# Performance work log

Hardware: AMD Instinct MI355X
Metric: run time of the kernel (lower is better)

The kernel has to match this reference:

```python
import jax, jax.numpy as jnp
import numpy as np
from jax import lax

K = 32768          # queue size
C = 100            # num_classes == len(cls_num_list1)
B = 1024           # batch size (features.shape[0] - K)
D = 128            # embedding dim
ALPHA = 0.05; BETA = 1.0; GAMMA = 1.0; SUPT = 1.0
T = 0.07; BASE_T = 0.07   # base_temperature defaults to temperature
SMOOTH = 0.0; EPS = 1e-12


def setup_inputs() -> dict:
    key = jax.random.key(0)
    k1, k2, k3, k4 = jax.random.split(key, 4)
    features = jax.random.normal(k1, (B + K, D), dtype=jnp.float32)
    features = features / jnp.linalg.norm(features, axis=1, keepdims=True)  # contrastive feats are L2-normalized
    centers = jax.random.normal(k2, (C, D), dtype=jnp.float32)
    centers = centers / jnp.linalg.norm(centers, axis=1, keepdims=True)
    sup_logits = jax.random.normal(k3, (B, C), dtype=jnp.float32)
    labels = jax.random.randint(k4, (B + K,), 0, C, dtype=jnp.int32)
    return {"features": features, "sup_logits": sup_logits, "centers": centers, "labels": labels}


def _loss(features, sup_logits, centers, labels):
    f32 = features.dtype
    lab_c = jnp.arange(C, dtype=labels.dtype)
    lab1 = jnp.concatenate([labels[:B], lab_c])                 # [B+C]
    mask = (labels[:B, None] == labels[None, :]).astype(f32)    # [B, B+K]
    mask1 = (lab1[:B, None] == lab1[None, :]).astype(f32)       # [B, B+C]
    # class counts over batch+queue (batch_cls_count) and batch+centers (batch_cls_count1)
    cls_count = jnp.zeros((C,), f32).at[labels].add(1.0)
    cls_count1 = jnp.zeros((C,), f32).at[lab1].add(1.0)
    diag = jnp.arange(B)
    logits_mask = jnp.ones((B, B + K), f32).at[diag, diag].set(0.0)
    logits_mask1 = jnp.ones((B, B + C), f32).at[diag, diag].set(0.0)
    mask = mask * logits_mask
    mask1 = mask1 * logits_mask1

    # ---- branch 1: batch anchors vs [batch, class centers] ----
    feats1 = jnp.concatenate([features[:B], centers], axis=0)   # [B+C, D]
    logits1 = (features[:B] @ feats1.T) / T                     # [B, B+C]
    logits1 = logits1 - lax.stop_gradient(logits1.max(axis=1, keepdims=True))
    exp1 = jnp.exp(logits1) * logits_mask1
    w1 = cls_count1[lab1][None, :] - mask1                      # per-instance class weight
    denom1 = (exp1 / w1).sum(axis=1, keepdims=True)
    log_prob1 = logits1 - jnp.log(denom1 + EPS)
    loss1 = -jnp.mean((mask1 * log_prob1).sum(1) / mask1.sum(1))

    # ---- branch 2: [sup_logits, batch anchors vs batch+queue] ----
    adc = (features[:B] @ features.T) / T                       # [B, B+K]
    logits = jnp.concatenate([sup_logits / SUPT, adc], axis=1)  # [B, C+B+K] (self.weight is None)
    logits = logits - lax.stop_gradient(logits.max(axis=1, keepdims=True))
    one_hot = jax.nn.one_hot(labels[:B], C, dtype=f32)
    one_hot = SMOOTH / (C - 1) * (1.0 - one_hot) + (1.0 - SMOOTH) * one_hot
    mask_full = jnp.concatenate([one_hot * BETA, mask * ALPHA], axis=1)
    lmask_full = jnp.concatenate([jnp.ones((B, C), f32), GAMMA * logits_mask], axis=1)
    expl = jnp.exp(logits) * lmask_full
    lab_full = jnp.concatenate([lab_c, labels])                 # [C+B+K]
    w = cls_count[lab_full][None, :] - mask_full
    denom = (expl / w).sum(axis=1, keepdims=True)
    log_prob = logits - jnp.log(denom + EPS)
    loss2 = -(T / BASE_T) * jnp.mean((mask_full * log_prob).sum(1) / mask_full.sum(1))
    return loss1 + loss2


def reference(features, sup_logits, centers, labels):
    return _loss(features, sup_logits, centers, labels)
```

## Files before the change

kernel.cpp:

```cpp
#include <hip/hip_runtime.h>
#include <math.h>

#define KQ   32768
#define CC   100
#define BB   1024
#define DD   128
#define NTOT (BB + KQ)
#define CB_CENT 1056
#define NCB  1060
#define NPB  265
#define NHIST 33
#define NCG2 66
#define CG_SUP 75
#define NSL  75

#define INV_T  14.285714285714286f
#define K2E    20.609929f
#define ALPHA  0.05f
#define EPSV   1e-12f

typedef __attribute__((ext_vector_type(8)))  short          short8;
typedef __attribute__((ext_vector_type(8)))  unsigned short ushort8;
typedef __attribute__((ext_vector_type(16))) float          float16;

__device__ __forceinline__ unsigned short f2bf_rne(float f) {
    unsigned int u = __float_as_uint(f);
    return (unsigned short)((u + 0x7FFFu + ((u >> 16) & 1u)) >> 16);
}


__global__ __launch_bounds__(256) void prep_k(const float* __restrict__ feats,
                                              const float* __restrict__ centers,
                                              const int* __restrict__ labels,
                                              unsigned short* __restrict__ X2,
                                              int* __restrict__ cntP,
                                              int* __restrict__ cntB) {
    const int b = blockIdx.x, t = threadIdx.x;
    if (b >= NPB) {
        const int h = b - NPB;
        __shared__ int hA[CC], hB[CC];
        if (t < CC) { hA[t] = 0; hB[t] = 0; }
        __syncthreads();
        const int base = h * 1024;
#pragma unroll
        for (int q = 0; q < 4; ++q) {
            int l = labels[base + q * 256 + t];
            atomicAdd(&hA[l], 1);
            if (h == 0) atomicAdd(&hB[l], 1);
        }
        __syncthreads();
        if (t < 128) {
            cntP[h * 128 + t] = (t < CC) ? hA[t] : 0;
            if (h == 0) cntB[t] = (t < CC) ? hB[t] : 0;
        }
        return;
    }
    __shared__ unsigned short sm[8 * 66 * 8];
    const int rl = t >> 3, c8 = t & 7;
#pragma unroll
    for (int cbi = 0; cbi < 4; ++cbi) {
        const int cb = b * 4 + cbi;
        if (cb >= NCB) break;
        const int r = cb * 32 + rl;
        const float* src;
        if (r < NTOT)            src = &feats[(size_t)r * DD];
        else if (r < NTOT + CC)  src = &centers[(size_t)(r - NTOT) * DD];
        else                     src = nullptr;
        if (cbi) __syncthreads();
#pragma unroll
        for (int s = 0; s < 2; ++s) {
            const int c8p = c8 + 8 * s;
            float v[8];
            if (src) {
                const float4* p = (const float4*)(src + c8p * 8);
                float4 q0 = p[0], q1 = p[1];
                v[0]=q0.x; v[1]=q0.y; v[2]=q0.z; v[3]=q0.w;
                v[4]=q1.x; v[5]=q1.y; v[6]=q1.z; v[7]=q1.w;
            } else {
#pragma unroll
                for (int j = 0; j < 8; ++j) v[j] = 0.f;
            }
            ushort8 H;
#pragma unroll
            for (int m = 0; m < 8; ++m) H[m] = f2bf_rne(v[m]);
            const int ks = c8p >> 1, lh = c8p & 1;
            *(ushort8*)&sm[(ks * 66 + rl + 32 * lh) * 8] = H;
        }
        __syncthreads();
        ushort8* dst = (ushort8*)((char*)X2 + (size_t)cb * 8192);
#pragma unroll
        for (int j = 0; j < 2; ++j) {
            const int idx = j * 256 + t;
            const int ks = idx >> 6, ln = idx & 63;
            dst[idx] = *(const ushort8*)&sm[(ks * 66 + ln) * 8];
        }
    }
}

__device__ __forceinline__ void epi_tile(
    const float16& acc, int cb, int lc, float rn, float drm, bool checkDiag,
    int half, int ln, int growbase, const int* rlab, float* sS, float* sN)
{
    const int ccol = cb * 32 + ln;
#pragma unroll
    for (int reg = 0; reg < 16; ++reg) {
        int ro = (reg & 3) + 8 * (reg >> 2) + 4 * half;
        float a  = acc[reg];
        float mf = (lc == rlab[reg]) ? 1.f : 0.f;
        float wgt = fmaf(mf, drm, rn);
        if (checkDiag) {
            bool d = (ccol == growbase + ro);
            wgt = d ? 0.f : wgt;
            mf  = d ? 0.f : mf;
        }
        float e = exp2f(fmaf(a, K2E, -K2E));
        sS[reg] = fmaf(e, wgt, sS[reg]);
        sN[reg] = fmaf(mf, a, sN[reg]);
    }
}

__device__ __forceinline__ void pair_tiles(
    const char* Xb, int cb0, int cb1,
    int lc0, float rn0, float drm0, bool dg0,
    int lc1, float rn1, float drm1, bool dg1,
    int lane, int half, int ln, int growbase,
    const short8* Ah, const int* rlab, float* sS, float* sN)
{
    const size_t b0 = (size_t)cb0 * 8192 + (size_t)lane * 16;
    const size_t b1 = (size_t)cb1 * 8192 + (size_t)lane * 16;
    float16 a0, a1;
#pragma unroll
    for (int reg = 0; reg < 16; ++reg) { a0[reg] = 0.f; a1[reg] = 0.f; }
#pragma unroll
    for (int ks = 0; ks < 8; ++ks) {
        short8 B0 = *(const short8*)(Xb + b0 + (size_t)ks * 1024);
        short8 B1 = *(const short8*)(Xb + b1 + (size_t)ks * 1024);
        a0 = __builtin_amdgcn_mfma_f32_32x32x16_bf16(Ah[ks], B0, a0, 0, 0, 0);
        a1 = __builtin_amdgcn_mfma_f32_32x32x16_bf16(Ah[ks], B1, a1, 0, 0, 0);
    }
    epi_tile(a0, cb0, lc0, rn0, drm0, dg0, half, ln, growbase, rlab, sS, sN);
    epi_tile(a1, cb1, lc1, rn1, drm1, dg1, half, ln, growbase, rlab, sS, sN);
}

__global__ __launch_bounds__(256) void gemm_k(
    const unsigned short* __restrict__ X2, const int* __restrict__ labels,
    const int* __restrict__ cntP, const int* __restrict__ cntB,
    const float* __restrict__ sup,
    float* __restrict__ pS, float* __restrict__ pN,
    float* __restrict__ supS, float* __restrict__ supLi) {
    const int b = blockIdx.x;
    const int xcd = b & 7, l = b >> 3;
    const int rt = l & 7, ci = l >> 3;
    const int cg = xcd + 8 * ci;
    if (cg > CG_SUP) return;

    const int tid = threadIdx.x;
    const int lane = tid & 63, w = tid >> 6;
    const int half = lane >> 5, ln = lane & 31;
    const char* Xb = (const char*)X2;

    __shared__ float cntAF[128], rnA[128], drmA[128], rn1S[128], drm1S[128];
    if (tid < 128) {
        int s = 0;
#pragma unroll
        for (int h = 0; h < NHIST; ++h) s += cntP[h * 128 + tid];
        float cf = (float)s;
        cntAF[tid] = cf;
        rnA[tid] = (s > 0) ? __builtin_amdgcn_rcpf(cf) : 0.f;
        drmA[tid] = (s > 0) ? (__builtin_amdgcn_rcpf(cf - ALPHA) - rnA[tid]) : 0.f;
        int sb = cntB[tid];
        float c1 = (float)(sb + 1);
        float rn1 = __builtin_amdgcn_rcpf(c1);
        rn1S[tid] = rn1;
        drm1S[tid] = __builtin_amdgcn_rcpf(fmaxf(c1 - 1.f, 1.f)) - rn1;
    }
    __syncthreads();

    if (cg == CG_SUP) {
        const int g = rt * 4 + w;
        const int c0 = lane, c1 = lane + 64;
        float n0 = cntAF[c0];
        float rA0 = __builtin_amdgcn_rcpf(n0);
        float rAm0 = __builtin_amdgcn_rcpf(fmaxf(n0 - 1.f, 1.f));
        float rA1 = 0.f, rAm1 = 0.f;
        if (lane < 36) {
            float n1 = cntAF[c1];
            rA1 = __builtin_amdgcn_rcpf(n1);
            rAm1 = __builtin_amdgcn_rcpf(fmaxf(n1 - 1.f, 1.f));
        }
        for (int rr = 0; rr < 32; ++rr) {
            int row = g * 32 + rr;
            int li = labels[row];
            const float* srow = &sup[(size_t)row * CC];
            float v0 = srow[c0];
            float s = __expf(v0 - INV_T) * ((c0 == li) ? rAm0 : rA0);
            float liv = (c0 == li) ? v0 : 0.f;
            if (lane < 36) {
                float v1 = srow[c1];
                s += __expf(v1 - INV_T) * ((c1 == li) ? rAm1 : rA1);
                liv += (c1 == li) ? v1 : 0.f;
            }
#pragma unroll
            for (int off = 1; off < 64; off <<= 1) {
                s += __shfl_xor(s, off, 64);
                liv += __shfl_xor(liv, off, 64);
            }
            if (lane == 0) { supS[row] = s; supLi[row] = liv; }
        }
        return;
    }

    const int rb = rt * 4 + w;
    const int growbase = rt * 128 + w * 32;
    short8 Ah[8];
    {
        size_t abase = (size_t)rb * 8192 + (size_t)lane * 16;
#pragma unroll
        for (int ks = 0; ks < 8; ++ks)
            Ah[ks] = *(const short8*)(Xb + abase + (size_t)ks * 1024);
    }
    int rlab[16];
#pragma unroll
    for (int reg = 0; reg < 16; ++reg) {
        int ro = (reg & 3) + 8 * (reg >> 2) + 4 * half;
        rlab[reg] = labels[growbase + ro];
    }
    float sS[16], sN[16];
#pragma unroll
    for (int reg = 0; reg < 16; ++reg) { sS[reg] = 0.f; sN[reg] = 0.f; }

    const bool isB2 = (cg < NCG2);
    const int t1 = cg - NCG2;
    if (isB2) {
#pragma unroll
        for (int p = 0; p < 8; ++p) {
            const int cb0 = cg * 16 + 2 * p, cb1 = cb0 + 1;
            int lc0 = labels[cb0 * 32 + ln];
            int lc1 = labels[cb1 * 32 + ln];
            pair_tiles(Xb, cb0, cb1, lc0, rnA[lc0], drmA[lc0], cb0 == rb,
                       lc1, rnA[lc1], drmA[lc1], cb1 == rb,
                       lane, half, ln, growbase, Ah, rlab, sS, sN);
        }
    } else {
        const bool isBatch = (t1 < 8);
#pragma unroll
        for (int p = 0; p < 2; ++p) {
            int cb0, cb1, lc0, lc1;
            if (isBatch) {
                cb0 = t1 * 4 + 2 * p; cb1 = cb0 + 1;
                lc0 = labels[cb0 * 32 + ln];
                lc1 = labels[cb1 * 32 + ln];
            } else {
                cb0 = CB_CENT + 2 * p; cb1 = cb0 + 1;
                int q0 = cb0 * 32 + ln - NTOT, q1 = cb1 * 32 + ln - NTOT;
                lc0 = (q0 < CC) ? q0 : -1;
                lc1 = (q1 < CC) ? q1 : -1;
            }
            float rn0 = (lc0 >= 0) ? rn1S[lc0] : 0.f;
            float drm0 = (lc0 >= 0) ? drm1S[lc0] : 0.f;
            float rn1 = (lc1 >= 0) ? rn1S[lc1] : 0.f;
            float drm1 = (lc1 >= 0) ? drm1S[lc1] : 0.f;
            pair_tiles(Xb, cb0, cb1, lc0, rn0, drm0, isBatch && (cb0 == rb),
                       lc1, rn1, drm1, isBatch && (cb1 == rb),
                       lane, half, ln, growbase, Ah, rlab, sS, sN);
        }
    }
    const int slice = isB2 ? cg : (NCG2 + t1);
#pragma unroll
    for (int reg = 0; reg < 16; ++reg) {
        float a = sS[reg], c = sN[reg];
#pragma unroll
        for (int off = 1; off < 32; off <<= 1) {
            a += __shfl_xor(a, off, 64);
            c += __shfl_xor(c, off, 64);
        }
        if (ln == 0) {
            int ro = (reg & 3) + 8 * (reg >> 2) + 4 * half;
            int grow = growbase + ro;
            pS[(size_t)slice * BB + grow] = a;
            pN[(size_t)slice * BB + grow] = c;
        }
    }
}

__global__ __launch_bounds__(1024) void finalize_k(
    const int* __restrict__ labels,
    const int* __restrict__ cntP, const int* __restrict__ cntB,
    const float* __restrict__ pS, const float* __restrict__ pN,
    const float* __restrict__ supS, const float* __restrict__ supLi,
    float* __restrict__ out) {
    const int t = threadIdx.x;
    __shared__ float cntA[128];
    if (t < 128) {
        int s = 0;
#pragma unroll
        for (int h = 0; h < NHIST; ++h) s += cntP[h * 128 + t];
        cntA[t] = (float)s;
    }
    __syncthreads();
    const int li = labels[t];
    float S2 = supS[t], N2 = 0.f;
#pragma unroll 4
    for (int c = 0; c < NCG2; ++c) {
        S2 += pS[(size_t)c * BB + t];
        N2 += pN[(size_t)c * BB + t];
    }
    float S1 = 0.f, N1v = 0.f;
#pragma unroll
    for (int c = NCG2; c < NSL; ++c) {
        S1 += pS[(size_t)c * BB + t];
        N1v += pN[(size_t)c * BB + t];
    }
    N2 *= INV_T; N1v *= INV_T;
    float sli = supLi[t];
    float cA = cntA[li];
    float msum2 = fmaf(ALPHA, cA - 1.f, 1.f);
    float loss2 = -(fmaf(ALPHA, N2, sli) / msum2 - INV_T - logf(S2 + EPSV));
    float loss1 = -(N1v / (float)cntB[li] - INV_T - logf(S1 + EPSV));
    float s = loss1 + loss2;
    __shared__ float buf[16];
#pragma unroll
    for (int off = 1; off < 64; off <<= 1) s += __shfl_xor(s, off, 64);
    if ((t & 63) == 0) buf[t >> 6] = s;
    __syncthreads();
    if (t < 64) {
        float x = (t < 16) ? buf[t] : 0.f;
#pragma unroll
        for (int off = 1; off < 16; off <<= 1) x += __shfl_xor(x, off, 64);
        if (t == 0) out[0] = x / (float)BB;
    }
}

extern "C" void kernel_launch(void* const* d_in, const int* in_sizes, int n_in,
                              void* d_out, int out_size, void* d_ws, size_t ws_size,
                              hipStream_t stream) {
    const float* feats   = (const float*)d_in[0];
    const float* sup     = (const float*)d_in[1];
    const float* centers = (const float*)d_in[2];
    const int*   labels  = (const int*)d_in[3];
    float* out = (float*)d_out;
    char*  wsb = (char*)d_ws;

    const size_t X2_BYTES = (size_t)NCB * 8192;
    unsigned short* X2 = (unsigned short*)wsb;
    char* base2 = wsb + X2_BYTES;
    int* cntP = (int*)base2;
    int* cntB = cntP + NHIST * 128;
    float* pS = (float*)(cntB + 128);
    float* pN = pS + (size_t)NSL * BB;
    float* supS  = pN + (size_t)NSL * BB;
    float* supLi = supS + BB;

    prep_k<<<NPB + NHIST, 256, 0, stream>>>(feats, centers, labels, X2, cntP, cntB);
    gemm_k<<<8 * 8 * 10, 256, 0, stream>>>(X2, labels, cntP, cntB, sup,
                                           pS, pN, supS, supLi);
    finalize_k<<<1, 1024, 0, stream>>>(labels, cntP, cntB, pS, pN, supS, supLi, out);
}
```

Before: 130.3 us.

## Split GEMM into single-wave blocks, add class-weight table kernel, one chunk per prep block

The prep kernel now converts one 32-row chunk per block instead of four, which launches more blocks. A new tiny kernel computes the per-class reciprocal weight tables once, so GEMM blocks no longer each re-sum the histogram partials and synchronise. The GEMM kernel uses 64-thread blocks, each covering one row block and half as many column tiles, which doubles the column groups and the partial-sum slices. The goal is better load balance and less redundant preamble work, at the cost of an extra launch, more partial sums for finalize to reduce, and no A-fragment reuse across waves in a block.

```diff
diff --git a/kernel.cpp b/kernel.cpp
--- a/kernel.cpp
+++ b/kernel.cpp
@@ -8,11 +8,11 @@
 #define NTOT (BB + KQ)
 #define CB_CENT 1056
 #define NCB  1060
-#define NPB  265
 #define NHIST 33
-#define NCG2 66
-#define CG_SUP 75
-#define NSL  75
+#define NCG2 132
+#define CG_SUP 141
+#define NSL  141
+#define NCI  18
 
 #define INV_T  14.285714285714286f
 #define K2E    20.609929f
@@ -36,8 +36,8 @@
                                               int* __restrict__ cntP,
                                               int* __restrict__ cntB) {
     const int b = blockIdx.x, t = threadIdx.x;
-    if (b >= NPB) {
-        const int h = b - NPB;
+    if (b >= NCB) {
+        const int h = b - NCB;
         __shared__ int hA[CC], hB[CC];
         if (t < CC) { hA[t] = 0; hB[t] = 0; }
         __syncthreads();
@@ -56,45 +56,62 @@
         return;
     }
     __shared__ unsigned short sm[8 * 66 * 8];
+    const int cb = b;
     const int rl = t >> 3, c8 = t & 7;
-#pragma unroll
-    for (int cbi = 0; cbi < 4; ++cbi) {
-        const int cb = b * 4 + cbi;
-        if (cb >= NCB) break;
-        const int r = cb * 32 + rl;
-        const float* src;
-        if (r < NTOT)            src = &feats[(size_t)r * DD];
-        else if (r < NTOT + CC)  src = &centers[(size_t)(r - NTOT) * DD];
-        else                     src = nullptr;
-        if (cbi) __syncthreads();
-#pragma unroll
-        for (int s = 0; s < 2; ++s) {
-            const int c8p = c8 + 8 * s;
-            float v[8];
-            if (src) {
-                const float4* p = (const float4*)(src + c8p * 8);
-                float4 q0 = p[0], q1 = p[1];
-                v[0]=q0.x; v[1]=q0.y; v[2]=q0.z; v[3]=q0.w;
-                v[4]=q1.x; v[5]=q1.y; v[6]=q1.z; v[7]=q1.w;
-            } else {
-#pragma unroll
-                for (int j = 0; j < 8; ++j) v[j] = 0.f;
-            }
-            ushort8 H;
-#pragma unroll
-            for (int m = 0; m < 8; ++m) H[m] = f2bf_rne(v[m]);
-            const int ks = c8p >> 1, lh = c8p & 1;
-            *(ushort8*)&sm[(ks * 66 + rl + 32 * lh) * 8] = H;
-        }
-        __syncthreads();
-        ushort8* dst = (ushort8*)((char*)X2 + (size_t)cb * 8192);
-#pragma unroll
-        for (int j = 0; j < 2; ++j) {
-            const int idx = j * 256 + t;
-            const int ks = idx >> 6, ln = idx & 63;
-            dst[idx] = *(const ushort8*)&sm[(ks * 66 + ln) * 8];
-        }
-    }
+    const int r = cb * 32 + rl;
+    const float* src;
+    if (r < NTOT)            src = &feats[(size_t)r * DD];
+    else if (r < NTOT + CC)  src = &centers[(size_t)(r - NTOT) * DD];
+    else                     src = nullptr;
+#pragma unroll
+    for (int s = 0; s < 2; ++s) {
+        const int c8p = c8 + 8 * s;
+        float v[8];
+        if (src) {
+            const float4* p = (const float4*)(src + c8p * 8);
+            float4 q0 = p[0], q1 = p[1];
+            v[0]=q0.x; v[1]=q0.y; v[2]=q0.z; v[3]=q0.w;
+            v[4]=q1.x; v[5]=q1.y; v[6]=q1.z; v[7]=q1.w;
+        } else {
+#pragma unroll
+            for (int j = 0; j < 8; ++j) v[j] = 0.f;
+        }
+        ushort8 H;
+#pragma unroll
+        for (int m = 0; m < 8; ++m) H[m] = f2bf_rne(v[m]);
+        const int ks = c8p >> 1, lh = c8p & 1;
+        *(ushort8*)&sm[(ks * 66 + rl + 32 * lh) * 8] = H;
+    }
+    __syncthreads();
+    ushort8* dst = (ushort8*)((char*)X2 + (size_t)cb * 8192);
+#pragma unroll
+    for (int j = 0; j < 2; ++j) {
+        const int idx = j * 256 + t;
+        const int ks = idx >> 6, ln2 = idx & 63;
+        dst[idx] = *(const ushort8*)&sm[(ks * 66 + ln2) * 8];
+    }
+}
+
+__global__ __launch_bounds__(128) void tables_k(
+    const int* __restrict__ cntP, const int* __restrict__ cntB,
+    float2* __restrict__ wA, float2* __restrict__ w1, float2* __restrict__ wS,
+    float* __restrict__ cAf, int* __restrict__ cBi) {
+    const int t = threadIdx.x;
+    int s = 0;
+#pragma unroll
+    for (int h = 0; h < NHIST; ++h) s += cntP[h * 128 + t];
+    float cf = (float)s;
+    float rn = (s > 0) ? __builtin_amdgcn_rcpf(cf) : 0.f;
+    float dr = (s > 0) ? (__builtin_amdgcn_rcpf(cf - ALPHA) - rn) : 0.f;
+    wA[t] = make_float2(rn, dr);
+    wS[t] = make_float2(__builtin_amdgcn_rcpf(cf),
+                        __builtin_amdgcn_rcpf(fmaxf(cf - 1.f, 1.f)));
+    int sb = cntB[t];
+    float c1 = (float)(sb + 1);
+    float r1 = __builtin_amdgcn_rcpf(c1);
+    w1[t] = make_float2(r1, __builtin_amdgcn_rcpf(fmaxf(c1 - 1.f, 1.f)) - r1);
+    cAf[t] = cf;
+    cBi[t] = sb;
 }
 
 __device__ __forceinline__ void epi_tile(
@@ -142,54 +159,30 @@
     epi_tile(a1, cb1, lc1, rn1, drm1, dg1, half, ln, growbase, rlab, sS, sN);
 }
 
-__global__ __launch_bounds__(256) void gemm_k(
+__global__ __launch_bounds__(64, 4) void gemm_k(
     const unsigned short* __restrict__ X2, const int* __restrict__ labels,
-    const int* __restrict__ cntP, const int* __restrict__ cntB,
-    const float* __restrict__ sup,
+    const float2* __restrict__ wA, const float2* __restrict__ w1,
+    const float2* __restrict__ wS, const float* __restrict__ sup,
     float* __restrict__ pS, float* __restrict__ pN,
     float* __restrict__ supS, float* __restrict__ supLi) {
     const int b = blockIdx.x;
-    const int xcd = b & 7, l = b >> 3;
-    const int rt = l & 7, ci = l >> 3;
+    const int xcd = b & 7, u = b >> 3;
+    const int ci = u >> 5, rb = u & 31;
     const int cg = xcd + 8 * ci;
     if (cg > CG_SUP) return;
 
-    const int tid = threadIdx.x;
-    const int lane = tid & 63, w = tid >> 6;
+    const int lane = threadIdx.x & 63;
     const int half = lane >> 5, ln = lane & 31;
     const char* Xb = (const char*)X2;
 
-    __shared__ float cntAF[128], rnA[128], drmA[128], rn1S[128], drm1S[128];
-    if (tid < 128) {
-        int s = 0;
-#pragma unroll
-        for (int h = 0; h < NHIST; ++h) s += cntP[h * 128 + tid];
-        float cf = (float)s;
-        cntAF[tid] = cf;
-        rnA[tid] = (s > 0) ? __builtin_amdgcn_rcpf(cf) : 0.f;
-        drmA[tid] = (s > 0) ? (__builtin_amdgcn_rcpf(cf - ALPHA) - rnA[tid]) : 0.f;
-        int sb = cntB[tid];
-        float c1 = (float)(sb + 1);
-        float rn1 = __builtin_amdgcn_rcpf(c1);
-        rn1S[tid] = rn1;
-        drm1S[tid] = __builtin_amdgcn_rcpf(fmaxf(c1 - 1.f, 1.f)) - rn1;
-    }
-    __syncthreads();
-
     if (cg == CG_SUP) {
-        const int g = rt * 4 + w;
         const int c0 = lane, c1 = lane + 64;
-        float n0 = cntAF[c0];
-        float rA0 = __builtin_amdgcn_rcpf(n0);
-        float rAm0 = __builtin_amdgcn_rcpf(fmaxf(n0 - 1.f, 1.f));
+        float2 t0 = wS[c0];
+        float rA0 = t0.x, rAm0 = t0.y;
         float rA1 = 0.f, rAm1 = 0.f;
-        if (lane < 36) {
-            float n1 = cntAF[c1];
-            rA1 = __builtin_amdgcn_rcpf(n1);
-            rAm1 = __builtin_amdgcn_rcpf(fmaxf(n1 - 1.f, 1.f));
-        }
+        if (lane < 36) { float2 t1 = wS[c1]; rA1 = t1.x; rAm1 = t1.y; }
         for (int rr = 0; rr < 32; ++rr) {
-            int row = g * 32 + rr;
+            int row = rb * 32 + rr;
             int li = labels[row];
             const float* srow = &sup[(size_t)row * CC];
             float v0 = srow[c0];
@@ -210,8 +203,7 @@
         return;
     }
 
-    const int rb = rt * 4 + w;
-    const int growbase = rt * 128 + w * 32;
+    const int growbase = rb * 32;
     short8 Ah[8];
     {
         size_t abase = (size_t)rb * 8192 + (size_t)lane * 16;
@@ -233,12 +225,13 @@
     const int t1 = cg - NCG2;
     if (isB2) {
 #pragma unroll
-        for (int p = 0; p < 8; ++p) {
-            const int cb0 = cg * 16 + 2 * p, cb1 = cb0 + 1;
+        for (int p = 0; p < 4; ++p) {
+            const int cb0 = cg * 8 + 2 * p, cb1 = cb0 + 1;
             int lc0 = labels[cb0 * 32 + ln];
             int lc1 = labels[cb1 * 32 + ln];
-            pair_tiles(Xb, cb0, cb1, lc0, rnA[lc0], drmA[lc0], cb0 == rb,
-                       lc1, rnA[lc1], drmA[lc1], cb1 == rb,
+            float2 wv0 = wA[lc0], wv1 = wA[lc1];
+            pair_tiles(Xb, cb0, cb1, lc0, wv0.x, wv0.y, cb0 == rb,
+                       lc1, wv1.x, wv1.y, cb1 == rb,
                        lane, half, ln, growbase, Ah, rlab, sS, sN);
         }
     } else {
@@ -256,12 +249,14 @@
                 lc0 = (q0 < CC) ? q0 : -1;
                 lc1 = (q1 < CC) ? q1 : -1;
             }
-            float rn0 = (lc0 >= 0) ? rn1S[lc0] : 0.f;
-            float drm0 = (lc0 >= 0) ? drm1S[lc0] : 0.f;
-            float rn1 = (lc1 >= 0) ? rn1S[lc1] : 0.f;
-            float drm1 = (lc1 >= 0) ? drm1S[lc1] : 0.f;
+            float2 wv0 = w1[(lc0 >= 0) ? lc0 : 0];
+            float2 wv1 = w1[(lc1 >= 0) ? lc1 : 0];
+            float rn0  = (lc0 >= 0) ? wv0.x : 0.f;
+            float drm0 = (lc0 >= 0) ? wv0.y : 0.f;
+            float rn1v  = (lc1 >= 0) ? wv1.x : 0.f;
+            float drm1v = (lc1 >= 0) ? wv1.y : 0.f;
             pair_tiles(Xb, cb0, cb1, lc0, rn0, drm0, isBatch && (cb0 == rb),
-                       lc1, rn1, drm1, isBatch && (cb1 == rb),
+                       lc1, rn1v, drm1v, isBatch && (cb1 == rb),
                        lane, half, ln, growbase, Ah, rlab, sS, sN);
         }
     }
@@ -285,18 +280,14 @@
 
 __global__ __launch_bounds__(1024) void finalize_k(
     const int* __restrict__ labels,
-    const int* __restrict__ cntP, const int* __restrict__ cntB,
+    const float* __restrict__ cAf, const int* __restrict__ cBi,
     const float* __restrict__ pS, const float* __restrict__ pN,
     const float* __restrict__ supS, const float* __restrict__ supLi,
     float* __restrict__ out) {
     const int t = threadIdx.x;
-    __shared__ float cntA[128];
-    if (t < 128) {
-        int s = 0;
-#pragma unroll
-        for (int h = 0; h < NHIST; ++h) s += cntP[h * 128 + t];
-        cntA[t] = (float)s;
-    }
+    __shared__ float cA_s[128];
+    __shared__ int   cB_s[128];
+    if (t < 128) { cA_s[t] = cAf[t]; cB_s[t] = cBi[t]; }
     __syncthreads();
     const int li = labels[t];
     float S2 = supS[t], N2 = 0.f;
@@ -313,10 +304,10 @@
     }
     N2 *= INV_T; N1v *= INV_T;
     float sli = supLi[t];
-    float cA = cntA[li];
+    float cA = cA_s[li];
     float msum2 = fmaf(ALPHA, cA - 1.f, 1.f);
     float loss2 = -(fmaf(ALPHA, N2, sli) / msum2 - INV_T - logf(S2 + EPSV));
-    float loss1 = -(N1v / (float)cntB[li] - INV_T - logf(S1 + EPSV));
+    float loss1 = -(N1v / (float)cB_s[li] - INV_T - logf(S1 + EPSV));
     float s = loss1 + loss2;
     __shared__ float buf[16];
 #pragma unroll
@@ -346,13 +337,19 @@
     char* base2 = wsb + X2_BYTES;
     int* cntP = (int*)base2;
     int* cntB = cntP + NHIST * 128;
-    float* pS = (float*)(cntB + 128);
+    float2* wA = (float2*)(cntB + 128);
+    float2* w1 = wA + 128;
+    float2* wS = w1 + 128;
+    float*  cAf = (float*)(wS + 128);
+    int*    cBi = (int*)(cAf + 128);
+    float* pS = (float*)(cBi + 128);
     float* pN = pS + (size_t)NSL * BB;
     float* supS  = pN + (size_t)NSL * BB;
     float* supLi = supS + BB;
 
-    prep_k<<<NPB + NHIST, 256, 0, stream>>>(feats, centers, labels, X2, cntP, cntB);
-    gemm_k<<<8 * 8 * 10, 256, 0, stream>>>(X2, labels, cntP, cntB, sup,
-                                           pS, pN, supS, supLi);
-    finalize_k<<<1, 1024, 0, stream>>>(labels, cntP, cntB, pS, pN, supS, supLi, out);
-}
+    prep_k<<<NCB + NHIST, 256, 0, stream>>>(feats, centers, labels, X2, cntP, cntB);
+    tables_k<<<1, 128, 0, stream>>>(cntP, cntB, wA, w1, wS, cAf, cBi);
+    gemm_k<<<8 * 32 * NCI, 64, 0, stream>>>(X2, labels, wA, w1, wS, sup,
+                                            pS, pN, supS, supLi);
+    finalize_k<<<1, 1024, 0, stream>>>(labels, cAf, cBi, pS, pN, supS, supLi, out);
+}
```

After: 155.1 us. +19.0%, slower.
